# Optimization experiments

Hardware: AMD Instinct MI355X
Metric: run time of the kernel (lower is better)

Reference implementation:

```python
import jax, jax.numpy as jnp
import numpy as np

SIZE = 512
ATTN = 64      # per-head attention_size
OUT = 64       # per-head output_size
HEADS = 8

def setup_inputs() -> dict:
    key = jax.random.key(0)
    ks = jax.random.split(key, 7)
    s = 0.02
    return {
        "x":  jax.random.normal(ks[0], (4, 2048, SIZE), dtype=jnp.float32),
        "Wq": jax.random.normal(ks[1], (SIZE, ATTN * HEADS), dtype=jnp.float32) * s,
        "bq": jax.random.normal(ks[2], (ATTN * HEADS,), dtype=jnp.float32) * s,
        "Wk": jax.random.normal(ks[3], (SIZE, ATTN), dtype=jnp.float32) * s,  # shared key, no bias
        "Wv": jax.random.normal(ks[4], (SIZE, OUT * HEADS), dtype=jnp.float32) * s,
        "bv": jax.random.normal(ks[5], (OUT * HEADS,), dtype=jnp.float32) * s,
    }

def reference(x, Wq, bq, Wk, Wv, bv):
    B, S, _ = x.shape
    q = (x @ Wq + bq).reshape(B, S, HEADS, ATTN)   # (B,S,H,A)
    k = x @ Wk                                      # (B,S,A) shared across heads
    v = (x @ Wv + bv).reshape(B, S, HEADS, OUT)     # (B,S,H,O)
    # NOTE: original divides by sqrt(seq_len), not sqrt(head_dim)
    scale = 1.0 / np.sqrt(S).astype(np.float32)
    scores = jnp.einsum("bqha,bka->bhqk", q, k) * scale  # (B,H,S,S)
    causal = jnp.tril(jnp.ones((S, S), dtype=bool))
    scores = jnp.where(causal, scores, -jnp.inf)
    attn = jax.nn.softmax(scores, axis=-1)
    out = jnp.einsum("bhqk,bkho->bqho", attn, v)    # (B,S,H,O)
    return out.reshape(B, S, HEADS * OUT)
```

## Files before the change

### kernel.cpp

```cpp
#include <hip/hip_runtime.h>
#include <math.h>


typedef _Float16 half8 __attribute__((ext_vector_type(8)));
typedef _Float16 half4 __attribute__((ext_vector_type(4)));
typedef float float4v __attribute__((ext_vector_type(4)));
typedef unsigned int u32;

#define SCL2E 0.031885926f

__device__ inline float4v mfma16(half8 a, half8 b, float4v c) {
    return __builtin_amdgcn_mfma_f32_16x16x32_f16(a, b, c, 0, 0, 0);
}
__device__ inline void load16(const _Float16* g, _Float16* l) {
    __builtin_amdgcn_global_load_lds((const __attribute__((address_space(1))) u32*)g,
                                     (__attribute__((address_space(3))) u32*)l, 16, 0, 0);
}

__global__ __launch_bounds__(256) void prep(
    const float* __restrict__ x, const float* __restrict__ Wq,
    const float* __restrict__ Wk, const float* __restrict__ Wv,
    _Float16* __restrict__ xh, _Float16* __restrict__ wqt,
    _Float16* __restrict__ wkt, _Float16* __restrict__ wvt) {
    const int bid = blockIdx.x;
    if (bid < 2048) {
        size_t base = (size_t)bid * 2048 + (size_t)threadIdx.x * 8;
        const float4* xp = (const float4*)(x + base);
        float4 f0 = xp[0], f1 = xp[1];
        half8 h = {(_Float16)f0.x, (_Float16)f0.y, (_Float16)f0.z, (_Float16)f0.w,
                   (_Float16)f1.x, (_Float16)f1.y, (_Float16)f1.z, (_Float16)f1.w};
        *(half8*)(xh + base) = h;
    } else {
        int r = bid - 2048;
        const float* W; _Float16* WT; int N, bx, by;
        if (r < 256)      { W = Wq; WT = wqt; N = 512; bx = r & 15; by = r >> 4; }
        else if (r < 288) { r -= 256; W = Wk; WT = wkt; N = 64;  bx = r & 1;  by = r >> 1; }
        else              { r -= 288; W = Wv; WT = wvt; N = 512; bx = r & 15; by = r >> 4; }
        __shared__ float T[32][33];
        const int tx = threadIdx.x & 31, ty = threadIdx.x >> 5;
        const int n0 = bx * 32, k0 = by * 32;
#pragma unroll
        for (int i = 0; i < 4; ++i)
            T[ty + 8 * i][tx] = W[(size_t)(k0 + ty + 8 * i) * N + n0 + tx];
        __syncthreads();
#pragma unroll
        for (int i = 0; i < 4; ++i)
            WT[(size_t)(n0 + ty + 8 * i) * 512 + k0 + tx] = (_Float16)T[tx][ty + 8 * i];
    }
}

__global__ __launch_bounds__(256) void qkv_gemm(
    const _Float16* __restrict__ xh,
    const _Float16* __restrict__ wqt, const _Float16* __restrict__ wkt,
    const _Float16* __restrict__ wvt,
    const float* __restrict__ bq, const float* __restrict__ bv,
    _Float16* __restrict__ q_ws, _Float16* __restrict__ kt_ws, _Float16* __restrict__ vt_ws) {
    __shared__ __align__(16) _Float16 Xs[8192];
    __shared__ __align__(16) _Float16 Ws[8192];

    const int m0 = blockIdx.x * 128;
    const int y = blockIdx.y;
    const _Float16* WT;
    if (y < 4)       { WT = wqt + (size_t)y * 128 * 512; }
    else if (y == 4) { WT = wkt; }
    else             { WT = wvt + (size_t)(y - 5) * 128 * 512; }

    const int tid = threadIdx.x;
    const int w = tid >> 6, lane = tid & 63, quad = lane >> 4, cl = lane & 15;
    const int lrow = lane >> 3;
    const int lgc = (lane & 7) ^ lrow;
    const _Float16* xg = xh + (size_t)(m0 + lrow) * 512 + lgc * 8;
    const _Float16* wg = WT + (size_t)lrow * 512 + lgc * 8;

    const int g0 = (quad ^ (cl & 7)) << 3;
    const int g1 = ((quad ^ 4) ^ (cl & 7)) << 3;

    float4v acc[2][8] = {};

    for (int ki = 0; ki < 8; ++ki) {
        const int kk = ki * 64;
        __syncthreads();
#pragma unroll
        for (int c = 0; c < 4; ++c) {
            int cc = w * 4 + c;
            load16(xg + (size_t)cc * 8 * 512 + kk, Xs + cc * 512);
        }
        if (y != 4) {
#pragma unroll
            for (int c = 0; c < 4; ++c) {
                int cc = w * 4 + c;
                load16(wg + (size_t)cc * 8 * 512 + kk, Ws + cc * 512);
            }
        } else {
#pragma unroll
            for (int c = 0; c < 2; ++c) {
                int cc = w * 2 + c;
                load16(wg + (size_t)cc * 8 * 512 + kk, Ws + cc * 512);
            }
        }
        __syncthreads();
        if (y != 4) {
#pragma unroll
            for (int c = 0; c < 2; ++c) {
                const int g = c ? g1 : g0;
#pragma unroll
                for (int s = 0; s < 2; ++s) {
                    half8 a = *(const half8*)(Xs + (w * 32 + s * 16 + cl) * 64 + g);
#pragma unroll
                    for (int j = 0; j < 8; ++j) {
                        half8 b = *(const half8*)(Ws + (j * 16 + cl) * 64 + g);
                        acc[s][j] = mfma16(a, b, acc[s][j]);
                    }
                }
            }
        } else {
#pragma unroll
            for (int c = 0; c < 2; ++c) {
                const int g = c ? g1 : g0;
#pragma unroll
                for (int s = 0; s < 2; ++s) {
                    half8 a = *(const half8*)(Xs + (w * 32 + s * 16 + cl) * 64 + g);
#pragma unroll
                    for (int j = 0; j < 4; ++j) {
                        half8 b = *(const half8*)(Ws + (j * 16 + cl) * 64 + g);
                        acc[s][j] = mfma16(a, b, acc[s][j]);
                    }
                }
            }
        }
    }

    if (y < 4) {
#pragma unroll
        for (int s = 0; s < 2; ++s)
#pragma unroll
            for (int j = 0; j < 8; ++j)
#pragma unroll
                for (int r = 0; r < 4; ++r) {
                    int lr = w * 32 + s * 16 + quad * 4 + r;
                    int col = y * 128 + j * 16 + cl;
                    q_ws[(size_t)(m0 + lr) * 512 + col] =
                        (_Float16)((acc[s][j][r] + bq[col]) * SCL2E);
                }
    } else if (y == 4) {
#pragma unroll
        for (int s = 0; s < 2; ++s)
#pragma unroll
            for (int j = 0; j < 4; ++j)
#pragma unroll
                for (int r = 0; r < 4; ++r) {
                    int grow = m0 + w * 32 + s * 16 + quad * 4 + r;
                    int b = grow >> 11, t = (grow >> 6) & 31, row = grow & 63;
                    int col = j * 16 + cl;
                    kt_ws[((size_t)(b * 32 + t) << 12) + row * 64 +
                          (((col >> 3) ^ (row & 7)) << 3) + (col & 7)] = (_Float16)acc[s][j][r];
                }
    } else {
#pragma unroll
        for (int s = 0; s < 2; ++s)
#pragma unroll
            for (int j = 0; j < 8; ++j)
#pragma unroll
                for (int r = 0; r < 4; ++r) {
                    int grow = m0 + w * 32 + s * 16 + quad * 4 + r;
                    int b = grow >> 11, t = (grow >> 6) & 31, row = grow & 63;
                    int h = (y - 5) * 2 + (j >> 2);
                    int o = (j & 3) * 16 + cl;
                    int kap = ((row & 15) << 2) + (row >> 4);
                    vt_ws[(((size_t)(b * 8 + h) * 32 + t) << 12) + o * 64 +
                          (((kap >> 3) ^ (o & 7)) << 3) + (kap & 7)] =
                        (_Float16)(acc[s][j][r] + bv[h * 64 + o]);
                }
    }
}

__global__ __launch_bounds__(512, 2) void attn(
    const _Float16* __restrict__ q_ws, const _Float16* __restrict__ kt_ws,
    const _Float16* __restrict__ vt_ws, float* __restrict__ out) {
    __shared__ __align__(16) _Float16 Ks[2][2][4096];
    __shared__ __align__(16) _Float16 VTs[2][2][4096];
    __shared__ __align__(16) _Float16 Ps[8][1024];

    const int bh = blockIdx.x, b = bh >> 3, h = bh & 7;
    const int p = 31 - blockIdx.y;
    const int q0 = p * 64;
    const int nmax = (p + 2) >> 1;

    const int bS = b * 2048;
    const int tid = threadIdx.x;
    const int w = tid >> 6, lane = tid & 63, quad = lane >> 4, cl = lane & 15;
    const int g = w >> 2, wl = w & 3;
    const int tbase = g ? nmax : 0;
    const int nit = g ? (p + 1 - nmax) : nmax;

    const _Float16* kbase = kt_ws + ((size_t)(b * 32) << 12);
    const _Float16* vbase = vt_ws + ((size_t)((b * 8 + h) * 32) << 12);

    const int g0 = (quad ^ (cl & 7)) << 3;
    const int g1 = ((quad ^ 4) ^ (cl & 7)) << 3;
    const int so0 = wl * 1024 + lane * 8;

    const _Float16* qbase = q_ws + (size_t)(bS + q0 + wl * 16 + cl) * 512 + h * 64;
    half8 qa0 = *(const half8*)(qbase + quad * 8);
    half8 qa1 = *(const half8*)(qbase + 32 + quad * 8);

    float4v oacc[4] = {};
    float l_run[4] = {0.f, 0.f, 0.f, 0.f};

    _Float16* KsG = &Ks[g][0][0];
    _Float16* VsG = &VTs[g][0][0];

    auto stageK = [&](int tile, int buf) {
        const _Float16* kt = kbase + ((size_t)tile << 12);
        load16(kt + so0,       KsG + buf * 4096 + wl * 1024);
        load16(kt + so0 + 512, KsG + buf * 4096 + wl * 1024 + 512);
    };
    auto stageV = [&](int tile, int buf) {
        const _Float16* vt = vbase + ((size_t)tile << 12);
        load16(vt + so0,       VsG + buf * 4096 + wl * 1024);
        load16(vt + so0 + 512, VsG + buf * 4096 + wl * 1024 + 512);
    };
    auto qk_sm = [&](int tg, int buf) {
        const _Float16* KB = KsG + buf * 4096;
        if (tg != p) {
            float4v sfr[4];
#pragma unroll
            for (int j = 0; j < 4; ++j) {
                const _Float16* kr = KB + (j * 16 + cl) * 64;
                half8 b0 = *(const half8*)(kr + g0);
                half8 b1 = *(const half8*)(kr + g1);
                float4v a_ = {0.f, 0.f, 0.f, 0.f};
                a_ = mfma16(qa0, b0, a_);
                a_ = mfma16(qa1, b1, a_);
                sfr[j] = a_;
            }
#pragma unroll
            for (int r = 0; r < 4; ++r) {
                float p0 = exp2f(sfr[0][r]), p1 = exp2f(sfr[1][r]);
                float p2 = exp2f(sfr[2][r]), p3 = exp2f(sfr[3][r]);
                l_run[r] += (p0 + p1) + (p2 + p3);
                int rr = quad * 4 + r;
                half4 ph = {(_Float16)p0, (_Float16)p1, (_Float16)p2, (_Float16)p3};
                *(half4*)&Ps[w][rr * 64 + ((((cl >> 1) ^ (rr & 7)) << 3) | ((cl & 1) << 2))] = ph;
            }
        } else {
            const int jmax = wl;
            float4v sfr[4];
#pragma unroll
            for (int j = 0; j < 4; ++j) {
                if (j <= jmax) {
                    const _Float16* kr = KB + (j * 16 + cl) * 64;
                    half8 b0 = *(const half8*)(kr + g0);
                    half8 b1 = *(const half8*)(kr + g1);
                    float4v a_ = {0.f, 0.f, 0.f, 0.f};
                    a_ = mfma16(qa0, b0, a_);
                    a_ = mfma16(qa1, b1, a_);
                    sfr[j] = a_;
                }
            }
#pragma unroll
            for (int r = 0; r < 4; ++r) {
                float pj[4];
#pragma unroll
                for (int j = 0; j < 4; ++j) {
                    bool live = (j < jmax) || (j == jmax && cl <= quad * 4 + r);
                    pj[j] = live ? exp2f(sfr[j][r]) : 0.f;
                }
                l_run[r] += (pj[0] + pj[1]) + (pj[2] + pj[3]);
                int rr = quad * 4 + r;
                half4 ph = {(_Float16)pj[0], (_Float16)pj[1], (_Float16)pj[2], (_Float16)pj[3]};
                *(half4*)&Ps[w][rr * 64 + ((((cl >> 1) ^ (rr & 7)) << 3) | ((cl & 1) << 2))] = ph;
            }
        }
    };
    auto pv = [&](int buf) {
        const _Float16* PB = &Ps[w][cl * 64];
        half8 pa0 = *(const half8*)(PB + g0);
        half8 pa1 = *(const half8*)(PB + g1);
        const _Float16* VB = VsG + buf * 4096;
#pragma unroll
        for (int jo = 0; jo < 4; ++jo) {
            const _Float16* vr = VB + (jo * 16 + cl) * 64;
            half8 v0 = *(const half8*)(vr + g0);
            half8 v1 = *(const half8*)(vr + g1);
            oacc[jo] = mfma16(pa0, v0, oacc[jo]);
            oacc[jo] = mfma16(pa1, v1, oacc[jo]);
        }
    };

    if (nit > 0) {
        stageK(tbase, 0);
        if (g == 0) stageV(tbase, 0);
    }

    for (int t = 0; t < nmax; ++t) {
        const int cb = t & 1, nb = cb ^ 1;
        __syncthreads();
        const int tg = tbase + t;
        if (g == 0) {
            if (t + 1 < nit) { stageK(tg + 1, nb); stageV(tg + 1, nb); }
            qk_sm(tg, cb);
            pv(cb);
        } else {
            if (t > 0 && t - 1 < nit) pv(nb);
            if (t + 1 < nit) stageK(tg + 1, nb);
            if (t < nit) {
                stageV(tg, cb);
                qk_sm(tg, cb);
            }
        }
    }

    __syncthreads();
    if (g == 1 && nit == nmax) pv((nmax - 1) & 1);

    float* Obuf = (float*)&Ks[1][0][0];
    float* Lbuf = (float*)&VTs[0][0][0];
    if (g == 1) {
#pragma unroll
        for (int jo = 0; jo < 4; ++jo)
#pragma unroll
            for (int r = 0; r < 4; ++r) {
                int row = wl * 16 + quad * 4 + r;
                Obuf[row * 64 + jo * 16 + cl] = oacc[jo][r];
            }
#pragma unroll
        for (int r = 0; r < 4; ++r) {
            int row = wl * 16 + quad * 4 + r;
            Lbuf[row * 16 + cl] = l_run[r];
        }
    }
    __syncthreads();
    if (g == 0) {
#pragma unroll
        for (int r = 0; r < 4; ++r) {
            int row = wl * 16 + quad * 4 + r;
            float l = l_run[r] + Lbuf[row * 16 + cl];
            l += __shfl_xor(l, 1);
            l += __shfl_xor(l, 2);
            l += __shfl_xor(l, 4);
            l += __shfl_xor(l, 8);
            float inv = 1.0f / l;
            float* op = out + (size_t)(bS + q0 + row) * 512 + h * 64 + cl;
            op[0]  = (oacc[0][r] + Obuf[row * 64 +      cl]) * inv;
            op[16] = (oacc[1][r] + Obuf[row * 64 + 16 + cl]) * inv;
            op[32] = (oacc[2][r] + Obuf[row * 64 + 32 + cl]) * inv;
            op[48] = (oacc[3][r] + Obuf[row * 64 + 48 + cl]) * inv;
        }
    }
}

extern "C" void kernel_launch(void* const* d_in, const int* in_sizes, int n_in,
                              void* d_out, int out_size, void* d_ws, size_t ws_size,
                              hipStream_t stream) {
    const float* x  = (const float*)d_in[0];
    const float* Wq = (const float*)d_in[1];
    const float* bq = (const float*)d_in[2];
    const float* Wk = (const float*)d_in[3];
    const float* Wv = (const float*)d_in[4];
    const float* bv = (const float*)d_in[5];
    float* out = (float*)d_out;

    char* ws = (char*)d_ws;
    _Float16* q_ws  = (_Float16*)(ws);
    _Float16* kt_ws = (_Float16*)(ws + 8388608);
    _Float16* vt_ws = (_Float16*)(ws + 9437184);
    _Float16* wqt   = (_Float16*)(ws + 17825792);
    _Float16* wkt   = (_Float16*)(ws + 18350080);
    _Float16* wvt   = (_Float16*)(ws + 18415616);
    _Float16* xh    = (_Float16*)(ws + 18939904);

    prep<<<dim3(2592), dim3(256), 0, stream>>>(x, Wq, Wk, Wv, xh, wqt, wkt, wvt);

    qkv_gemm<<<dim3(64, 9), dim3(256), 0, stream>>>(
        xh, wqt, wkt, wvt, bq, bv, q_ws, kt_ws, vt_ws);

    attn<<<dim3(32, 32), dim3(512), 0, stream>>>(q_ws, kt_ws, vt_ws, out);
}
```

Baseline: 147.1 us.

## Double-buffer QKV GEMM LDS tiles with a 32-wide K step

The QKV projection GEMM now splits its LDS tiles into two buffers and halves the K-tile to 32. The next tile's async global-to-LDS load is issued right after the barrier, before the MFMAs on the current buffer, so loads overlap compute and each iteration needs one barrier instead of two. The XOR swizzle is reworked for the narrower 32-element rows. In exchange the loop runs twice as many iterations with less MFMA work per barrier, and the new swizzle may change LDS bank-conflict behaviour.

```diff
diff --git a/kernel.cpp b/kernel.cpp
--- a/kernel.cpp
+++ b/kernel.cpp
@@ -55,8 +55,8 @@
     const _Float16* __restrict__ wvt,
     const float* __restrict__ bq, const float* __restrict__ bv,
     _Float16* __restrict__ q_ws, _Float16* __restrict__ kt_ws, _Float16* __restrict__ vt_ws) {
-    __shared__ __align__(16) _Float16 Xs[8192];
-    __shared__ __align__(16) _Float16 Ws[8192];
+    __shared__ __align__(16) _Float16 Xs[2][4096];
+    __shared__ __align__(16) _Float16 Ws[2][4096];
 
     const int m0 = blockIdx.x * 128;
     const int y = blockIdx.y;
@@ -64,68 +64,54 @@
     if (y < 4)       { WT = wqt + (size_t)y * 128 * 512; }
     else if (y == 4) { WT = wkt; }
     else             { WT = wvt + (size_t)(y - 5) * 128 * 512; }
+    const int wcn = (y == 4) ? 4 : 8;
 
     const int tid = threadIdx.x;
     const int w = tid >> 6, lane = tid & 63, quad = lane >> 4, cl = lane & 15;
-    const int lrow = lane >> 3;
-    const int lgc = (lane & 7) ^ lrow;
+    const int lrow = lane >> 2;
+    const int lgc = (lane & 3) ^ (lrow & 3);
     const _Float16* xg = xh + (size_t)(m0 + lrow) * 512 + lgc * 8;
     const _Float16* wg = WT + (size_t)lrow * 512 + lgc * 8;
 
-    const int g0 = (quad ^ (cl & 7)) << 3;
-    const int g1 = ((quad ^ 4) ^ (cl & 7)) << 3;
+    const int ga = (quad ^ (cl & 3)) << 3;
 
     float4v acc[2][8] = {};
 
-    for (int ki = 0; ki < 8; ++ki) {
-        const int kk = ki * 64;
+    auto stage = [&](int kk, int buf) {
+#pragma unroll
+        for (int c = 0; c < 2; ++c) {
+            int cc = w * 2 + c;
+            load16(xg + (size_t)cc * 16 * 512 + kk, Xs[buf] + cc * 512);
+        }
+#pragma unroll
+        for (int c = 0; c < 2; ++c) {
+            int cc = w * 2 + c;
+            if (cc < wcn)
+                load16(wg + (size_t)cc * 16 * 512 + kk, Ws[buf] + cc * 512);
+        }
+    };
+
+    stage(0, 0);
+
+    for (int ki = 0; ki < 16; ++ki) {
+        const int cb = ki & 1, nb = cb ^ 1;
         __syncthreads();
-#pragma unroll
-        for (int c = 0; c < 4; ++c) {
-            int cc = w * 4 + c;
-            load16(xg + (size_t)cc * 8 * 512 + kk, Xs + cc * 512);
-        }
+        if (ki < 15) stage((ki + 1) * 32, nb);
+        half8 a0 = *(const half8*)(Xs[cb] + (w * 32 + cl) * 32 + ga);
+        half8 a1 = *(const half8*)(Xs[cb] + (w * 32 + 16 + cl) * 32 + ga);
         if (y != 4) {
 #pragma unroll
-            for (int c = 0; c < 4; ++c) {
-                int cc = w * 4 + c;
-                load16(wg + (size_t)cc * 8 * 512 + kk, Ws + cc * 512);
+            for (int j = 0; j < 8; ++j) {
+                half8 b = *(const half8*)(Ws[cb] + (j * 16 + cl) * 32 + ga);
+                acc[0][j] = mfma16(a0, b, acc[0][j]);
+                acc[1][j] = mfma16(a1, b, acc[1][j]);
             }
         } else {
 #pragma unroll
-            for (int c = 0; c < 2; ++c) {
-                int cc = w * 2 + c;
-                load16(wg + (size_t)cc * 8 * 512 + kk, Ws + cc * 512);
-            }
-        }
-        __syncthreads();
-        if (y != 4) {
-#pragma unroll
-            for (int c = 0; c < 2; ++c) {
-                const int g = c ? g1 : g0;
-#pragma unroll
-                for (int s = 0; s < 2; ++s) {
-                    half8 a = *(const half8*)(Xs + (w * 32 + s * 16 + cl) * 64 + g);
-#pragma unroll
-                    for (int j = 0; j < 8; ++j) {
-                        half8 b = *(const half8*)(Ws + (j * 16 + cl) * 64 + g);
-                        acc[s][j] = mfma16(a, b, acc[s][j]);
-                    }
-                }
-            }
-        } else {
-#pragma unroll
-            for (int c = 0; c < 2; ++c) {
-                const int g = c ? g1 : g0;
-#pragma unroll
-                for (int s = 0; s < 2; ++s) {
-                    half8 a = *(const half8*)(Xs + (w * 32 + s * 16 + cl) * 64 + g);
-#pragma unroll
-                    for (int j = 0; j < 4; ++j) {
-                        half8 b = *(const half8*)(Ws + (j * 16 + cl) * 64 + g);
-                        acc[s][j] = mfma16(a, b, acc[s][j]);
-                    }
-                }
+            for (int j = 0; j < 4; ++j) {
+                half8 b = *(const half8*)(Ws[cb] + (j * 16 + cl) * 32 + ga);
+                acc[0][j] = mfma16(a0, b, acc[0][j]);
+                acc[1][j] = mfma16(a1, b, acc[1][j]);
             }
         }
     }
```

Result: no change. 148.0 us (+0.6%).
